# Kernel optimization log

Hardware: AMD Instinct MI355X
Metric: run time of the kernel (lower is better)

Reference implementation:

```python
import jax, jax.numpy as jnp
import numpy as np

DIM = 256
HEADS = 8
HEAD_DIM = DIM // HEADS
SCALE = HEAD_DIM ** -0.5
EPS = 1e-5


def layer_norm(x, w, b):
    mu = jnp.mean(x, axis=-1, keepdims=True)
    var = jnp.mean(jnp.square(x - mu), axis=-1, keepdims=True)
    return (x - mu) * jax.lax.rsqrt(var + EPS) * w + b


def setup_inputs() -> dict:
    key = jax.random.key(0)
    ks = jax.random.split(key, 12)
    B, C, H, W = 2, DIM, 64, 64
    q_feat = jax.random.normal(ks[0], (B, C, H, W), dtype=jnp.float32)
    kv_feat = jax.random.normal(ks[1], (B, C, H, W), dtype=jnp.float32)
    s = 0.02
    return {
        "q_feat": q_feat,
        "kv_feat": kv_feat,
        "norm_q_w": jnp.ones((C,), jnp.float32),
        "norm_q_b": jnp.zeros((C,), jnp.float32),
        "norm_kv_w": jnp.ones((C,), jnp.float32),
        "norm_kv_b": jnp.zeros((C,), jnp.float32),
        "wq": jax.random.normal(ks[2], (C, C), jnp.float32) * s,
        "bq": jnp.zeros((C,), jnp.float32),
        "wk": jax.random.normal(ks[3], (C, C), jnp.float32) * s,
        "bk": jnp.zeros((C,), jnp.float32),
        "wv": jax.random.normal(ks[4], (C, C), jnp.float32) * s,
        "bv": jnp.zeros((C,), jnp.float32),
        "wp": jax.random.normal(ks[5], (C, C), jnp.float32) * s,
        "bp": jnp.zeros((C,), jnp.float32),
    }


def reference(q_feat, kv_feat, norm_q_w, norm_q_b, norm_kv_w, norm_kv_b,
              wq, bq, wk, bk, wv, bv, wp, bp):
    B, C, H, W = q_feat.shape
    N = H * W
    # N > max_tokens(256) -> avg_pool2d(k=2,s=2) on kv (H,W even so no ceil padding)
    kv = kv_feat.reshape(B, C, H // 2, 2, W // 2, 2).mean(axis=(3, 5))
    Hk, Wk = kv.shape[2], kv.shape[3]
    Nk = Hk * Wk
    q = q_feat.transpose(0, 2, 3, 1).reshape(B, N, C)
    kv = kv.transpose(0, 2, 3, 1).reshape(B, Nk, C)
    q = layer_norm(q, norm_q_w, norm_q_b)
    kv = layer_norm(kv, norm_kv_w, norm_kv_b)
    # projections (weights stored as (out,in) like torch Linear: x @ W.T + b)
    qh = (q @ wq.T + bq).reshape(B, N, HEADS, HEAD_DIM).transpose(0, 2, 1, 3)
    kh = (kv @ wk.T + bk).reshape(B, Nk, HEADS, HEAD_DIM).transpose(0, 2, 1, 3)
    vh = (kv @ wv.T + bv).reshape(B, Nk, HEADS, HEAD_DIM).transpose(0, 2, 1, 3)
    attn = jnp.einsum("bhnd,bhmd->bhnm", qh * SCALE, kh)
    attn = jax.nn.softmax(attn, axis=-1)
    out = jnp.einsum("bhnm,bhmd->bhnd", attn, vh)
    out = out.transpose(0, 2, 1, 3).reshape(B, N, C)
    out = out @ wp.T + bp
    return out.reshape(B, H, W, C).transpose(0, 3, 1, 2)
```

## Files before the change

kernel.cpp:

```cpp
#include <hip/hip_runtime.h>


#define CDIM   256
#define NTOK   4096
#define NKTOK  1024
#define HDIM   32
#define QSCALE 0.2550530290582177f
#define LN_EPS 1e-5f

typedef __attribute__((ext_vector_type(8))) short bf16x8;
typedef __attribute__((ext_vector_type(4))) float f32x4;

__device__ __forceinline__ ushort f2bf(float f) {
  uint u = __builtin_bit_cast(uint, f);
  u += 0x7fff + ((u >> 16) & 1);
  return (ushort)(u >> 16);
}

__device__ __forceinline__ float fast_exp2(float x) {
  float r;
  asm("v_exp_f32 %0, %1" : "=v"(r) : "v"(x));
  return r;
}

__device__ __forceinline__ void gload_lds16(const void* g, void* l) {
  __builtin_amdgcn_global_load_lds(
      (const __attribute__((address_space(1))) unsigned int*)g,
      (__attribute__((address_space(3))) unsigned int*)l, 16, 0, 0);
}

__global__ __launch_bounds__(256) void prep_kernel(
    const float* __restrict__ q_feat, const float* __restrict__ kv_feat,
    const float* __restrict__ nqw, const float* __restrict__ nqb,
    const float* __restrict__ nkw, const float* __restrict__ nkb,
    const float* __restrict__ wq, const float* __restrict__ wk,
    const float* __restrict__ wvv, const float* __restrict__ wp,
    ushort* __restrict__ wq_bf, ushort* __restrict__ wk_bf,
    ushort* __restrict__ wv_bf, ushort* __restrict__ wp_bf,
    ushort* __restrict__ q_ln, ushort* __restrict__ kv_ln) {
  __shared__ float preds[2][256];
  __shared__ float pstat[2][32];
  const int bid = blockIdx.x;
  const int tid = threadIdx.x;

  if (bid < 256) {
    const int mat = bid >> 6;
    const int base = (bid & 63) * 1024 + tid * 4;
    const float* s; ushort* d;
    switch (mat) {
      case 0: s = wq; d = wq_bf; break;
      case 1: s = wk; d = wk_bf; break;
      case 2: s = wvv; d = wv_bf; break;
      default: s = wp; d = wp_bf; break;
    }
    const float4 v = *reinterpret_cast<const float4*>(s + base);
    uint2 pk;
    pk.x = (uint)f2bf(v.x) | ((uint)f2bf(v.y) << 16);
    pk.y = (uint)f2bf(v.z) | ((uint)f2bf(v.w) << 16);
    *reinterpret_cast<uint2*>(d + base) = pk;
    return;
  }

  if (bid < 768) {
    const int tok = tid & 15, cg = tid >> 4;
    const int T = (bid - 256) * 16 + tok;
    const int b = T >> 12, n = T & 4095;
    const float* src = q_feat + ((size_t)b * CDIM + cg * 16) * NTOK + n;
    float vals[16];
    float s = 0.f, ss = 0.f;
#pragma unroll
    for (int ci = 0; ci < 16; ++ci) {
      const float v = src[(size_t)ci * NTOK];
      vals[ci] = v;
      s += v; ss = fmaf(v, v, ss);
    }
    preds[0][cg * 16 + tok] = s;
    preds[1][cg * 16 + tok] = ss;
    __syncthreads();
    if (tid < 16) {
      float st = 0.f, sst = 0.f;
#pragma unroll
      for (int k = 0; k < 16; ++k) { st += preds[0][k * 16 + tid]; sst += preds[1][k * 16 + tid]; }
      const float mu = st * (1.f / 256.f);
      const float var = sst * (1.f / 256.f) - mu * mu;
      pstat[0][tid] = mu;
      pstat[1][tid] = rsqrtf(var + LN_EPS);
    }
    __syncthreads();
    const float mu = pstat[0][tok];
    const float rs = pstat[1][tok];
    ushort* dst = q_ln + (size_t)T * CDIM + cg * 16;
#pragma unroll
    for (int ci = 0; ci < 16; ci += 4) {
      ushort h[4];
#pragma unroll
      for (int j = 0; j < 4; ++j) {
        const int c = cg * 16 + ci + j;
        h[j] = f2bf(fmaf((vals[ci + j] - mu) * rs, nqw[c], nqb[c]));
      }
      uint2 pk;
      pk.x = (uint)h[0] | ((uint)h[1] << 16);
      pk.y = (uint)h[2] | ((uint)h[3] << 16);
      *reinterpret_cast<uint2*>(dst + ci) = pk;
    }
    return;
  }

  {
    const int tok = tid & 7, cg = tid >> 3;
    const int T = (bid - 768) * 8 + tok;
    const int b = T >> 10, nk = T & 1023;
    const int hk = nk >> 5, wk2 = nk & 31;
    const float* src = kv_feat + ((size_t)b * CDIM + cg * 8) * NTOK + hk * 128 + wk2 * 2;
    float vals[8];
    float s = 0.f, ss = 0.f;
#pragma unroll
    for (int ci = 0; ci < 8; ++ci) {
      const float* p = src + (size_t)ci * NTOK;
      const float2 r0 = *reinterpret_cast<const float2*>(p);
      const float2 r1 = *reinterpret_cast<const float2*>(p + 64);
      const float v = 0.25f * ((r0.x + r0.y) + (r1.x + r1.y));
      vals[ci] = v;
      s += v; ss = fmaf(v, v, ss);
    }
    preds[0][cg * 8 + tok] = s;
    preds[1][cg * 8 + tok] = ss;
    __syncthreads();
    if (tid < 8) {
      float st = 0.f, sst = 0.f;
#pragma unroll
      for (int k = 0; k < 32; ++k) { st += preds[0][k * 8 + tid]; sst += preds[1][k * 8 + tid]; }
      const float mu = st * (1.f / 256.f);
      const float var = sst * (1.f / 256.f) - mu * mu;
      pstat[0][tid] = mu;
      pstat[1][tid] = rsqrtf(var + LN_EPS);
    }
    __syncthreads();
    const float mu = pstat[0][tok];
    const float rs = pstat[1][tok];
    ushort* dst = kv_ln + (size_t)T * CDIM + cg * 8;
#pragma unroll
    for (int ci = 0; ci < 8; ci += 4) {
      ushort h[4];
#pragma unroll
      for (int j = 0; j < 4; ++j) {
        const int c = cg * 8 + ci + j;
        h[j] = f2bf(fmaf((vals[ci + j] - mu) * rs, nkw[c], nkb[c]));
      }
      uint2 pk;
      pk.x = (uint)h[0] | ((uint)h[1] << 16);
      pk.y = (uint)h[2] | ((uint)h[3] << 16);
      *reinterpret_cast<uint2*>(dst + ci) = pk;
    }
  }
}

__global__ __launch_bounds__(256) void qkv_kernel(
    const ushort* __restrict__ q_ln, const ushort* __restrict__ kv_ln,
    const ushort* __restrict__ wq_bf, const ushort* __restrict__ wk_bf,
    const ushort* __restrict__ wv_bf,
    const float* __restrict__ bq, const float* __restrict__ bk,
    const float* __restrict__ bv,
    ushort* __restrict__ Qp, ushort* __restrict__ Kp, ushort* __restrict__ Vt) {
  const int bid = blockIdx.x;
  int seg, sb;
  const ushort *X, *W; const float* bias;
  if (bid < 256)      { seg = 0; sb = bid;       X = q_ln;  W = wq_bf; bias = bq; }
  else if (bid < 320) { seg = 1; sb = bid - 256; X = kv_ln; W = wk_bf; bias = bk; }
  else                { seg = 2; sb = bid - 320; X = kv_ln; W = wv_bf; bias = bv; }

  const int lane = threadIdx.x & 63;
  const int wvi = threadIdx.x >> 6;
  const int nlan = lane & 15, g = lane >> 4;
  const int rowgrp = wvi >> 1, colh = wvi & 1;
  const int r0 = sb * 32 + rowgrp * 16;

  f32x4 acc[8];
#pragma unroll
  for (int nt = 0; nt < 8; ++nt) acc[nt] = (f32x4){0.f, 0.f, 0.f, 0.f};

  const ushort* xp = X + (size_t)(r0 + nlan) * CDIM + g * 8;
  const ushort* wp = W + (size_t)(colh * 128 + nlan) * CDIM + g * 8;
#pragma unroll
  for (int k0 = 0; k0 < 8; ++k0) {
    const bf16x8 a = *reinterpret_cast<const bf16x8*>(xp + k0 * 32);
#pragma unroll
    for (int nt = 0; nt < 8; ++nt) {
      const bf16x8 bfr = *reinterpret_cast<const bf16x8*>(wp + (size_t)nt * 16 * CDIM + k0 * 32);
      acc[nt] = __builtin_amdgcn_mfma_f32_16x16x32_bf16(a, bfr, acc[nt], 0, 0, 0);
    }
  }

#pragma unroll
  for (int nt = 0; nt < 8; ++nt) {
    const int j = colh * 128 + nt * 16 + nlan;
    const float bj = bias[j];
#pragma unroll
    for (int reg = 0; reg < 4; ++reg) {
      const int r = r0 + 4 * g + reg;
      const float v = acc[nt][reg] + bj;
      if (seg == 0) {
        Qp[(size_t)r * CDIM + j] = f2bf(v * QSCALE);
      } else if (seg == 1) {
        Kp[(size_t)r * CDIM + j] = f2bf(v);
      } else {
        const int h = j >> 5, d = j & 31;
        const int bb = r >> 10, m = r & 1023;
        Vt[((size_t)((bb * 8 + h) * 32 + d)) * NKTOK + m] = f2bf(v);
      }
    }
  }
}

__global__ __launch_bounds__(256) void attn_kernel(const ushort* __restrict__ Qp,
                                                   const ushort* __restrict__ Kp,
                                                   const ushort* __restrict__ Vt,
                                                   ushort* __restrict__ aout) {
  __shared__ __align__(16) ushort kvf[2][16][512];
  __shared__ __align__(16) ushort P_lds[4][16][136];
  const int lane = threadIdx.x & 63;
  const int wvi = threadIdx.x >> 6;
  const int nlan = lane & 15, g = lane >> 4;
  const int bh = blockIdx.y;
  const int b = bh >> 3, h = bh & 7;
  const int n0 = blockIdx.x * 128 + wvi * 32;

  bf16x8 qf[2];
#pragma unroll
  for (int qt = 0; qt < 2; ++qt)
    qf[qt] = *reinterpret_cast<const bf16x8*>(
        Qp + (size_t)(b * NTOK + n0 + qt * 16 + nlan) * CDIM + h * HDIM + g * 8);

  const ushort* kb = Kp + (size_t)b * NKTOK * CDIM + h * HDIM;
  const ushort* vb = Vt + (size_t)(b * 8 + h) * HDIM * NKTOK;

  auto stage = [&](int buf, int kc) {
#pragma unroll
    for (int i = 0; i < 4; ++i) {
      const int t = wvi * 4 + i;
      const ushort* src;
      if (t < 8) {
        src = kb + (size_t)(kc + t * 16 + nlan) * CDIM + g * 8;
      } else {
        const int j = t - 8, dt = j >> 2, ks = j & 3;
        src = vb + (size_t)(dt * 16 + nlan) * NKTOK + kc + ks * 32 + g * 8;
      }
      gload_lds16(src, &kvf[buf][t][0]);
    }
  };

  f32x4 acc[2][2];
  f32x4 lsum[2];
#pragma unroll
  for (int qt = 0; qt < 2; ++qt) {
    lsum[qt] = (f32x4){0.f, 0.f, 0.f, 0.f};
#pragma unroll
    for (int dt = 0; dt < 2; ++dt) acc[qt][dt] = (f32x4){0.f, 0.f, 0.f, 0.f};
  }
  const f32x4 zero = {0.f, 0.f, 0.f, 0.f};

  stage(0, 0);
  for (int c = 0; c < 8; ++c) {
    const int buf = c & 1;
    __syncthreads();
    if (c < 7) stage(buf ^ 1, (c + 1) * 128);

#pragma unroll
    for (int qt = 0; qt < 2; ++qt) {
#pragma unroll
      for (int kt = 0; kt < 8; ++kt) {
        const bf16x8 kf = *reinterpret_cast<const bf16x8*>(&kvf[buf][kt][lane * 8]);
        const f32x4 s = __builtin_amdgcn_mfma_f32_16x16x32_bf16(qf[qt], kf, zero, 0, 0, 0);
#pragma unroll
        for (int reg = 0; reg < 4; ++reg) {
          const float p = fast_exp2(s[reg]);
          lsum[qt][reg] += p;
          P_lds[wvi][4 * g + reg][kt * 16 + nlan] = f2bf(p);
        }
      }
#pragma unroll
      for (int dt = 0; dt < 2; ++dt) {
#pragma unroll
        for (int ks = 0; ks < 4; ++ks) {
          const bf16x8 pa = *reinterpret_cast<const bf16x8*>(&P_lds[wvi][nlan][ks * 32 + g * 8]);
          const bf16x8 vf = *reinterpret_cast<const bf16x8*>(&kvf[buf][8 + dt * 4 + ks][lane * 8]);
          acc[qt][dt] = __builtin_amdgcn_mfma_f32_16x16x32_bf16(pa, vf, acc[qt][dt], 0, 0, 0);
        }
      }
    }
  }

#pragma unroll
  for (int qt = 0; qt < 2; ++qt) {
#pragma unroll
    for (int off = 1; off < 16; off <<= 1) {
#pragma unroll
      for (int reg = 0; reg < 4; ++reg) lsum[qt][reg] += __shfl_xor(lsum[qt][reg], off, 64);
    }
  }

  ushort* dst = aout + (size_t)(b * NTOK + n0) * CDIM + h * HDIM;
#pragma unroll
  for (int qt = 0; qt < 2; ++qt) {
#pragma unroll
    for (int reg = 0; reg < 4; ++reg) {
      const float inv = 1.f / lsum[qt][reg];
      const size_t row = (size_t)(qt * 16 + 4 * g + reg) * CDIM;
      dst[row + nlan] = f2bf(acc[qt][0][reg] * inv);
      dst[row + 16 + nlan] = f2bf(acc[qt][1][reg] * inv);
    }
  }
}

__global__ __launch_bounds__(256) void outproj_kernel(const ushort* __restrict__ A,
                                                      const ushort* __restrict__ W,
                                                      const float* __restrict__ bias,
                                                      float* __restrict__ out) {
  __shared__ float ts[256][33];
  const int lane = threadIdx.x & 63;
  const int wvi = threadIdx.x >> 6;
  const int nlan = lane & 15, g = lane >> 4;
  const int rowgrp = wvi >> 1, colh = wvi & 1;
  const int r0b = blockIdx.x * 32;
  const int r0 = r0b + rowgrp * 16;

  f32x4 acc[8];
#pragma unroll
  for (int nt = 0; nt < 8; ++nt) acc[nt] = (f32x4){0.f, 0.f, 0.f, 0.f};

  const ushort* xp = A + (size_t)(r0 + nlan) * CDIM + g * 8;
  const ushort* wp = W + (size_t)(colh * 128 + nlan) * CDIM + g * 8;
#pragma unroll
  for (int k0 = 0; k0 < 8; ++k0) {
    const bf16x8 a = *reinterpret_cast<const bf16x8*>(xp + k0 * 32);
#pragma unroll
    for (int nt = 0; nt < 8; ++nt) {
      const bf16x8 bfr = *reinterpret_cast<const bf16x8*>(wp + (size_t)nt * 16 * CDIM + k0 * 32);
      acc[nt] = __builtin_amdgcn_mfma_f32_16x16x32_bf16(a, bfr, acc[nt], 0, 0, 0);
    }
  }

#pragma unroll
  for (int nt = 0; nt < 8; ++nt) {
    const int j = colh * 128 + nt * 16 + nlan;
    const float bj = bias[j];
#pragma unroll
    for (int reg = 0; reg < 4; ++reg)
      ts[j][rowgrp * 16 + 4 * g + reg] = acc[nt][reg] + bj;
  }
  __syncthreads();
  const int b = r0b >> 12;
  const int n0g = r0b & 4095;
#pragma unroll
  for (int k = 0; k < 32; ++k) {
    const int idx = k * 256 + threadIdx.x;
    const int cl = idx >> 5, tok = idx & 31;
    out[((size_t)b * CDIM + cl) * NTOK + n0g + tok] = ts[cl][tok];
  }
}

extern "C" void kernel_launch(void* const* d_in, const int* in_sizes, int n_in,
                              void* d_out, int out_size, void* d_ws, size_t ws_size,
                              hipStream_t stream) {
  (void)in_sizes; (void)n_in; (void)out_size; (void)ws_size;
  const float* q_feat  = (const float*)d_in[0];
  const float* kv_feat = (const float*)d_in[1];
  const float* nqw = (const float*)d_in[2];
  const float* nqb = (const float*)d_in[3];
  const float* nkw = (const float*)d_in[4];
  const float* nkb = (const float*)d_in[5];
  const float* wq  = (const float*)d_in[6];
  const float* bq  = (const float*)d_in[7];
  const float* wk  = (const float*)d_in[8];
  const float* bk  = (const float*)d_in[9];
  const float* wv  = (const float*)d_in[10];
  const float* bv  = (const float*)d_in[11];
  const float* wp  = (const float*)d_in[12];
  const float* bp  = (const float*)d_in[13];
  float* out = (float*)d_out;

  ushort* p = (ushort*)d_ws;
  ushort* wq_bf = p; p += 65536;
  ushort* wk_bf = p; p += 65536;
  ushort* wv_bf = p; p += 65536;
  ushort* wp_bf = p; p += 65536;
  ushort* q_ln  = p; p += 8192 * 256;
  ushort* kv_ln = p; p += 2048 * 256;
  ushort* Qp    = p; p += 8192 * 256;
  ushort* Kp    = p; p += 2048 * 256;
  ushort* Vt    = p; p += 2048 * 256;
  ushort* aout  = p; p += 8192 * 256;

  prep_kernel<<<1024, 256, 0, stream>>>(q_feat, kv_feat, nqw, nqb, nkw, nkb,
                                        wq, wk, wv, wp,
                                        wq_bf, wk_bf, wv_bf, wp_bf, q_ln, kv_ln);
  qkv_kernel<<<384, 256, 0, stream>>>(q_ln, kv_ln, wq_bf, wk_bf, wv_bf,
                                      bq, bk, bv, Qp, Kp, Vt);
  attn_kernel<<<dim3(32, 16), 256, 0, stream>>>(Qp, Kp, Vt, aout);
  outproj_kernel<<<256, 256, 0, stream>>>(aout, wp_bf, bp, out);
}
```

Baseline: 75.72 us.

## Keep softmax probabilities in registers by computing transposed scores S^T

Computes the score MFMA with K as the A operand so each lane holds probabilities for one query across keys, then packs them with v_cvt_pk_bf16 directly into the A-operand fragment for the PV MFMA. This removes the per-wave P_lds shared-memory round trip and its write/read traffic. K rows are staged in a permuted order so the register layout matches the PV operand. Row sums become per-lane scalars reduced with two shuffles plus a broadcast shuffle at the end.

```diff
diff --git a/kernel.cpp b/kernel.cpp
--- a/kernel.cpp
+++ b/kernel.cpp
@@ -10,6 +10,7 @@
 
 typedef __attribute__((ext_vector_type(8))) short bf16x8;
 typedef __attribute__((ext_vector_type(4))) float f32x4;
+typedef __attribute__((ext_vector_type(4))) uint u32x4;
 
 __device__ __forceinline__ ushort f2bf(float f) {
   uint u = __builtin_bit_cast(uint, f);
@@ -20,6 +21,12 @@
 __device__ __forceinline__ float fast_exp2(float x) {
   float r;
   asm("v_exp_f32 %0, %1" : "=v"(r) : "v"(x));
+  return r;
+}
+
+__device__ __forceinline__ uint cvt_pk_bf16(float lo, float hi) {
+  uint r;
+  asm("v_cvt_pk_bf16_f32 %0, %1, %2" : "=v"(r) : "v"(lo), "v"(hi));
   return r;
 }
 
@@ -217,7 +224,6 @@
                                                    const ushort* __restrict__ Vt,
                                                    ushort* __restrict__ aout) {
   __shared__ __align__(16) ushort kvf[2][16][512];
-  __shared__ __align__(16) ushort P_lds[4][16][136];
   const int lane = threadIdx.x & 63;
   const int wvi = threadIdx.x >> 6;
   const int nlan = lane & 15, g = lane >> 4;
@@ -240,7 +246,8 @@
       const int t = wvi * 4 + i;
       const ushort* src;
       if (t < 8) {
-        src = kb + (size_t)(kc + t * 16 + nlan) * CDIM + g * 8;
+        const int krow = kc + (t >> 1) * 32 + (nlan >> 2) * 8 + (t & 1) * 4 + (nlan & 3);
+        src = kb + (size_t)krow * CDIM + g * 8;
       } else {
         const int j = t - 8, dt = j >> 2, ks = j & 3;
         src = vb + (size_t)(dt * 16 + nlan) * NKTOK + kc + ks * 32 + g * 8;
@@ -250,13 +257,12 @@
   };
 
   f32x4 acc[2][2];
-  f32x4 lsum[2];
 #pragma unroll
   for (int qt = 0; qt < 2; ++qt) {
-    lsum[qt] = (f32x4){0.f, 0.f, 0.f, 0.f};
-#pragma unroll
-    for (int dt = 0; dt < 2; ++dt) acc[qt][dt] = (f32x4){0.f, 0.f, 0.f, 0.f};
-  }
+    acc[qt][0] = (f32x4){0.f, 0.f, 0.f, 0.f};
+    acc[qt][1] = (f32x4){0.f, 0.f, 0.f, 0.f};
+  }
+  float lsum[2] = {0.f, 0.f};
   const f32x4 zero = {0.f, 0.f, 0.f, 0.f};
 
   stage(0, 0);
@@ -266,37 +272,41 @@
     if (c < 7) stage(buf ^ 1, (c + 1) * 128);
 
 #pragma unroll
-    for (int qt = 0; qt < 2; ++qt) {
-#pragma unroll
-      for (int kt = 0; kt < 8; ++kt) {
-        const bf16x8 kf = *reinterpret_cast<const bf16x8*>(&kvf[buf][kt][lane * 8]);
-        const f32x4 s = __builtin_amdgcn_mfma_f32_16x16x32_bf16(qf[qt], kf, zero, 0, 0, 0);
-#pragma unroll
-        for (int reg = 0; reg < 4; ++reg) {
-          const float p = fast_exp2(s[reg]);
-          lsum[qt][reg] += p;
-          P_lds[wvi][4 * g + reg][kt * 16 + nlan] = f2bf(p);
+    for (int m = 0; m < 4; ++m) {
+      uint pk[2][4];
+#pragma unroll
+      for (int half = 0; half < 2; ++half) {
+        const bf16x8 kf = *reinterpret_cast<const bf16x8*>(&kvf[buf][2 * m + half][lane * 8]);
+#pragma unroll
+        for (int qt = 0; qt < 2; ++qt) {
+          const f32x4 s = __builtin_amdgcn_mfma_f32_16x16x32_bf16(kf, qf[qt], zero, 0, 0, 0);
+          const float p0 = fast_exp2(s[0]), p1 = fast_exp2(s[1]);
+          const float p2 = fast_exp2(s[2]), p3 = fast_exp2(s[3]);
+          lsum[qt] += (p0 + p1) + (p2 + p3);
+          pk[qt][half * 2 + 0] = cvt_pk_bf16(p0, p1);
+          pk[qt][half * 2 + 1] = cvt_pk_bf16(p2, p3);
         }
       }
+      bf16x8 af[2];
+#pragma unroll
+      for (int qt = 0; qt < 2; ++qt) {
+        const u32x4 w = {pk[qt][0], pk[qt][1], pk[qt][2], pk[qt][3]};
+        af[qt] = __builtin_bit_cast(bf16x8, w);
+      }
 #pragma unroll
       for (int dt = 0; dt < 2; ++dt) {
-#pragma unroll
-        for (int ks = 0; ks < 4; ++ks) {
-          const bf16x8 pa = *reinterpret_cast<const bf16x8*>(&P_lds[wvi][nlan][ks * 32 + g * 8]);
-          const bf16x8 vf = *reinterpret_cast<const bf16x8*>(&kvf[buf][8 + dt * 4 + ks][lane * 8]);
-          acc[qt][dt] = __builtin_amdgcn_mfma_f32_16x16x32_bf16(pa, vf, acc[qt][dt], 0, 0, 0);
-        }
+        const bf16x8 vf = *reinterpret_cast<const bf16x8*>(&kvf[buf][8 + dt * 4 + m][lane * 8]);
+#pragma unroll
+        for (int qt = 0; qt < 2; ++qt)
+          acc[qt][dt] = __builtin_amdgcn_mfma_f32_16x16x32_bf16(af[qt], vf, acc[qt][dt], 0, 0, 0);
       }
     }
   }
 
 #pragma unroll
   for (int qt = 0; qt < 2; ++qt) {
-#pragma unroll
-    for (int off = 1; off < 16; off <<= 1) {
-#pragma unroll
-      for (int reg = 0; reg < 4; ++reg) lsum[qt][reg] += __shfl_xor(lsum[qt][reg], off, 64);
-    }
+    lsum[qt] += __shfl_xor(lsum[qt], 16);
+    lsum[qt] += __shfl_xor(lsum[qt], 32);
   }
 
   ushort* dst = aout + (size_t)(b * NTOK + n0) * CDIM + h * HDIM;
@@ -304,7 +314,7 @@
   for (int qt = 0; qt < 2; ++qt) {
 #pragma unroll
     for (int reg = 0; reg < 4; ++reg) {
-      const float inv = 1.f / lsum[qt][reg];
+      const float inv = 1.f / __shfl(lsum[qt], 4 * g + reg);
       const size_t row = (size_t)(qt * 16 + 4 * g + reg) * CDIM;
       dst[row + nlan] = f2bf(acc[qt][0][reg] * inv);
       dst[row + 16 + nlan] = f2bf(acc[qt][1][reg] * inv);
```

Result: faster. 64.98 us (-14.2%).
